# Optimization experiments

Hardware: AMD Instinct MI355X
Metric: run time of the kernel (lower is better)

Reference implementation:

```python
import jax, jax.numpy as jnp
import numpy as np

B, N, IN, OUT = 16, 1000, 128, 128


def setup_inputs() -> dict:
    key = jax.random.key(0)
    ks = jax.random.split(key, 8)
    stdv = 1.0 / np.sqrt(IN + OUT)  # matches reset_param uniform(-stdv, stdv)
    def w(k):
        return jax.random.uniform(k, (N, IN + OUT, OUT), jnp.float32, -stdv, stdv)
    return {
        "xt": jax.random.normal(ks[0], (B, N, IN), jnp.float32),
        "hidden": jax.random.normal(ks[1], (1, N, OUT), jnp.float32),
        "ct_1": jax.random.normal(ks[2], (1, N, OUT), jnp.float32),
        "W_i": w(ks[3]), "b_i": jnp.zeros((N, OUT), jnp.float32),
        "W_o": w(ks[4]), "b_o": jnp.zeros((N, OUT), jnp.float32),
        "W_f": w(ks[5]), "b_f": jnp.zeros((N, OUT), jnp.float32),
        "W_c": w(ks[6]), "b_c": jnp.zeros((N, OUT), jnp.float32),
    }


def reference(xt, hidden, ct_1, W_i, b_i, W_o, b_o, W_f, b_f, W_c, b_c):
    b = xt.shape[0]
    h = jnp.broadcast_to(hidden, (b,) + hidden.shape[1:])       # [B,N,OUT]
    xh = jnp.concatenate([xt, h], axis=-1)                      # [B,N,IN+OUT]

    def gate(W, bias, act):
        # per-stock batched matmul: [B,N,K] x [N,K,O] -> [B,N,O]
        return act(jnp.einsum('bnk,nko->bno', xh, W) + bias)

    it = gate(W_i, b_i, jax.nn.sigmoid)
    ot = gate(W_o, b_o, jax.nn.sigmoid)
    ft = gate(W_f, b_f, jax.nn.sigmoid)
    chat = gate(W_c, b_c, jnp.tanh)

    ct = ft * jnp.broadcast_to(ct_1, it.shape) + it * chat
    ht = ot * jnp.tanh(ct)
    return ht, ct
```

## Files before the change

### kernel.cpp

```cpp
#include <hip/hip_runtime.h>
#include <hip/hip_bf16.h>

namespace {
constexpr int B   = 16;
constexpr int NS  = 1000;
constexpr int IN  = 128;
constexpr int OUT = 128;
constexpr int K   = 256;

typedef __attribute__((ext_vector_type(8))) short short8;
typedef __attribute__((ext_vector_type(4))) float f32x4;

__device__ __forceinline__ float fsigmoid(float x) {
  return 1.0f / (1.0f + __expf(-x));
}
__device__ __forceinline__ float ftanh(float x) {
  return 2.0f / (1.0f + __expf(-2.0f * x)) - 1.0f;
}
__device__ __forceinline__ unsigned int f2bf(float f) {
  unsigned int u = __builtin_bit_cast(unsigned int, f);
  u += 0x7fffu + ((u >> 16) & 1u);
  return u >> 16;
}
__device__ __forceinline__ unsigned int pack2(float lo, float hi) {
  return f2bf(lo) | (f2bf(hi) << 16);
}
__device__ __forceinline__ int slice_addr(int base, int kq, int col) {
  return base + (kq << 10) + ((col << 4) ^ (((col >> 3) & 7) << 4));
}

__global__ __launch_bounds__(512, 2) void lstm_kernel(
    const float* __restrict__ xt, const float* __restrict__ hidden,
    const float* __restrict__ ct_1,
    const float* __restrict__ Wi, const float* __restrict__ bi,
    const float* __restrict__ Wo, const float* __restrict__ bo,
    const float* __restrict__ Wf, const float* __restrict__ bfp,
    const float* __restrict__ Wc, const float* __restrict__ bc,
    float* __restrict__ out) {
  __shared__ __align__(16) unsigned char smem[40960];

  const int n   = blockIdx.x;
  const int tid = threadIdx.x;

  {
    const int b  = tid >> 5;
    const int s  = tid & 31;
    const int k0 = s << 3;
    float v[8];
    if (k0 < IN) {
      const float4 a = *reinterpret_cast<const float4*>(xt + ((size_t)b * NS + n) * IN + k0);
      const float4 c = *reinterpret_cast<const float4*>(xt + ((size_t)b * NS + n) * IN + k0 + 4);
      v[0]=a.x; v[1]=a.y; v[2]=a.z; v[3]=a.w; v[4]=c.x; v[5]=c.y; v[6]=c.z; v[7]=c.w;
    } else {
      const float4 a = *reinterpret_cast<const float4*>(hidden + (size_t)n * OUT + (k0 - IN));
      const float4 c = *reinterpret_cast<const float4*>(hidden + (size_t)n * OUT + (k0 - IN) + 4);
      v[0]=a.x; v[1]=a.y; v[2]=a.z; v[3]=a.w; v[4]=c.x; v[5]=c.y; v[6]=c.z; v[7]=c.w;
    }
    uint4 pk;
    pk.x = pack2(v[0], v[1]); pk.y = pack2(v[2], v[3]);
    pk.z = pack2(v[4], v[5]); pk.w = pack2(v[6], v[7]);
    const int addr = ((b << 9) + (s << 4)) ^ ((b & 7) << 4);
    *reinterpret_cast<uint4*>(&smem[addr]) = pk;
  }
  __syncthreads();

  const int wid  = tid >> 6;
  const int g    = wid >> 1;
  const int half = wid & 1;
  const int l    = tid & 63;
  const int g2   = l >> 4;
  const int c16  = l & 15;

  const float* Wg = (g == 0) ? Wi : (g == 1) ? Wo : (g == 2) ? Wf : Wc;
  const float* bg = (g == 0) ? bi : (g == 1) ? bo : (g == 2) ? bfp : bc;
  const float* wbase = Wg + (size_t)n * (K * OUT) + half * 64 + (c16 << 2);

  const int wsl = 8192 + (wid << 12);
  f32x4 acc[4] = {f32x4{0,0,0,0}, f32x4{0,0,0,0}, f32x4{0,0,0,0}, f32x4{0,0,0,0}};

  float4 wqa[8], wqb[8];
  #pragma unroll
  for (int i = 0; i < 8; ++i)
    wqa[i] = *reinterpret_cast<const float4*>(wbase + (size_t)((g2 << 3) + i) * OUT);
  #pragma unroll
  for (int i = 0; i < 8; ++i)
    wqb[i] = *reinterpret_cast<const float4*>(wbase + (size_t)(32 + (g2 << 3) + i) * OUT);

  #pragma unroll 1
  for (int c = 0; c < 8; c += 2) {
    {
      uint4 pk[4];
      #pragma unroll
      for (int j = 0; j < 4; ++j) {
        pk[j].x = pack2((&wqa[0].x)[j], (&wqa[1].x)[j]);
        pk[j].y = pack2((&wqa[2].x)[j], (&wqa[3].x)[j]);
        pk[j].z = pack2((&wqa[4].x)[j], (&wqa[5].x)[j]);
        pk[j].w = pack2((&wqa[6].x)[j], (&wqa[7].x)[j]);
      }
      const int cn = (c + 2 < 8) ? c + 2 : 0;
      #pragma unroll
      for (int i = 0; i < 8; ++i)
        wqa[i] = *reinterpret_cast<const float4*>(
            wbase + (size_t)((cn << 5) + (g2 << 3) + i) * OUT);
      #pragma unroll
      for (int j = 0; j < 4; ++j)
        *reinterpret_cast<uint4*>(&smem[slice_addr(wsl, g2, (c16 << 2) + j)]) = pk[j];

      const int aaddr = ((c16 << 9) + (c << 6) + (g2 << 4)) ^ ((c16 & 7) << 4);
      const short8 af = *reinterpret_cast<const short8*>(&smem[aaddr]);
      #pragma unroll
      for (int t = 0; t < 4; ++t) {
        const short8 bfv = *reinterpret_cast<const short8*>(
            &smem[slice_addr(wsl, g2, (t << 4) + c16)]);
        acc[t] = __builtin_amdgcn_mfma_f32_16x16x32_bf16(af, bfv, acc[t], 0, 0, 0);
      }
    }
    {
      uint4 pk[4];
      #pragma unroll
      for (int j = 0; j < 4; ++j) {
        pk[j].x = pack2((&wqb[0].x)[j], (&wqb[1].x)[j]);
        pk[j].y = pack2((&wqb[2].x)[j], (&wqb[3].x)[j]);
        pk[j].z = pack2((&wqb[4].x)[j], (&wqb[5].x)[j]);
        pk[j].w = pack2((&wqb[6].x)[j], (&wqb[7].x)[j]);
      }
      const int cn = (c + 3 < 8) ? c + 3 : 0;
      #pragma unroll
      for (int i = 0; i < 8; ++i)
        wqb[i] = *reinterpret_cast<const float4*>(
            wbase + (size_t)((cn << 5) + (g2 << 3) + i) * OUT);
      #pragma unroll
      for (int j = 0; j < 4; ++j)
        *reinterpret_cast<uint4*>(&smem[slice_addr(wsl, g2, (c16 << 2) + j)]) = pk[j];

      const int aaddr = ((c16 << 9) + ((c + 1) << 6) + (g2 << 4)) ^ ((c16 & 7) << 4);
      const short8 af = *reinterpret_cast<const short8*>(&smem[aaddr]);
      #pragma unroll
      for (int t = 0; t < 4; ++t) {
        const short8 bfv = *reinterpret_cast<const short8*>(
            &smem[slice_addr(wsl, g2, (t << 4) + c16)]);
        acc[t] = __builtin_amdgcn_mfma_f32_16x16x32_bf16(af, bfv, acc[t], 0, 0, 0);
      }
    }
  }

  __syncthreads();
  float* gb = reinterpret_cast<float*>(smem);
  #pragma unroll
  for (int t = 0; t < 4; ++t) {
    const int colg = (half << 6) + (t << 4) + c16;
    const float bias = bg[(size_t)n * OUT + colg];
    #pragma unroll
    for (int r = 0; r < 4; ++r) {
      const int b = (g2 << 2) + r;
      gb[g * 2064 + b * 129 + colg] = acc[t][r] + bias;
    }
  }
  __syncthreads();

  const size_t nbase = (size_t)n * OUT;
  #pragma unroll
  for (int r = 0; r < 4; ++r) {
    const int p = tid + (r << 9);
    const int b = p >> 7;
    const int o = p & 127;
    const float gi = gb[0 * 2064 + b * 129 + o];
    const float go = gb[1 * 2064 + b * 129 + o];
    const float gf = gb[2 * 2064 + b * 129 + o];
    const float gc = gb[3 * 2064 + b * 129 + o];
    const float it = fsigmoid(gi);
    const float ot = fsigmoid(go);
    const float ft = fsigmoid(gf);
    const float ch = ftanh(gc);
    const float cp = ct_1[nbase + o];
    const float ct = ft * cp + it * ch;
    const float ht = ot * ftanh(ct);
    const size_t oidx = (size_t)b * ((size_t)NS * OUT) + nbase + o;
    out[oidx] = ht;
    out[(size_t)B * NS * OUT + oidx] = ct;
  }
}
}

extern "C" void kernel_launch(void* const* d_in, const int* in_sizes, int n_in,
                              void* d_out, int out_size, void* d_ws, size_t ws_size,
                              hipStream_t stream) {
  const float* xt     = (const float*)d_in[0];
  const float* hidden = (const float*)d_in[1];
  const float* ct_1   = (const float*)d_in[2];
  const float* Wi     = (const float*)d_in[3];
  const float* bi     = (const float*)d_in[4];
  const float* Wo     = (const float*)d_in[5];
  const float* bo     = (const float*)d_in[6];
  const float* Wf     = (const float*)d_in[7];
  const float* bf     = (const float*)d_in[8];
  const float* Wc     = (const float*)d_in[9];
  const float* bc     = (const float*)d_in[10];

  lstm_kernel<<<NS, 512, 0, stream>>>(xt, hidden, ct_1, Wi, bi, Wo, bo,
                                      Wf, bf, Wc, bc,
                                      (float*)d_out);
}
```

Before: 110.6 us.

## Split each stock across two 256-thread blocks by output half

Each stock is now handled by two blocks, one per 64-column half of the output, with four waves (one per gate) instead of eight. The weight prefetch per step is halved: each wave loads 32 K-rows per iteration in two 16-row halves and does one MFMA step per iteration. Shared memory shrinks to 24 KB and launch bounds allow six blocks per CU, aiming for more occupancy and more blocks in flight to hide weight-streaming latency. In exchange, the activation tile (xt and hidden) is loaded and converted twice per stock, and each iteration now carries less independent memory work.

```diff
diff --git a/kernel.cpp b/kernel.cpp
--- a/kernel.cpp
+++ b/kernel.cpp
@@ -29,7 +29,7 @@
   return base + (kq << 10) + ((col << 4) ^ (((col >> 3) & 7) << 4));
 }
 
-__global__ __launch_bounds__(512, 2) void lstm_kernel(
+__global__ __launch_bounds__(256, 6) void lstm_kernel(
     const float* __restrict__ xt, const float* __restrict__ hidden,
     const float* __restrict__ ct_1,
     const float* __restrict__ Wi, const float* __restrict__ bi,
@@ -37,15 +37,19 @@
     const float* __restrict__ Wf, const float* __restrict__ bfp,
     const float* __restrict__ Wc, const float* __restrict__ bc,
     float* __restrict__ out) {
-  __shared__ __align__(16) unsigned char smem[40960];
+  __shared__ __align__(16) unsigned char smem[24576];
 
-  const int n   = blockIdx.x;
-  const int tid = threadIdx.x;
+  const int bid  = blockIdx.x;
+  const int n    = bid >> 1;
+  const int half = bid & 1;
+  const int tid  = threadIdx.x;
 
-  {
-    const int b  = tid >> 5;
-    const int s  = tid & 31;
-    const int k0 = s << 3;
+  #pragma unroll
+  for (int r = 0; r < 2; ++r) {
+    const int idx = tid + (r << 8);
+    const int b   = idx >> 5;
+    const int s   = idx & 31;
+    const int k0  = s << 3;
     float v[8];
     if (k0 < IN) {
       const float4 a = *reinterpret_cast<const float4*>(xt + ((size_t)b * NS + n) * IN + k0);
@@ -64,83 +68,73 @@
   }
   __syncthreads();
 
-  const int wid  = tid >> 6;
-  const int g    = wid >> 1;
-  const int half = wid & 1;
-  const int l    = tid & 63;
-  const int g2   = l >> 4;
-  const int c16  = l & 15;
+  const int g   = tid >> 6;
+  const int l   = tid & 63;
+  const int g2  = l >> 4;
+  const int c16 = l & 15;
 
   const float* Wg = (g == 0) ? Wi : (g == 1) ? Wo : (g == 2) ? Wf : Wc;
   const float* bg = (g == 0) ? bi : (g == 1) ? bo : (g == 2) ? bfp : bc;
   const float* wbase = Wg + (size_t)n * (K * OUT) + half * 64 + (c16 << 2);
 
-  const int wsl = 8192 + (wid << 12);
+  const int wsl = 8192 + (g << 12);
   f32x4 acc[4] = {f32x4{0,0,0,0}, f32x4{0,0,0,0}, f32x4{0,0,0,0}, f32x4{0,0,0,0}};
 
-  float4 wqa[8], wqb[8];
+  float4 wqa[4], wqb[4];
   #pragma unroll
-  for (int i = 0; i < 8; ++i)
-    wqa[i] = *reinterpret_cast<const float4*>(wbase + (size_t)((g2 << 3) + i) * OUT);
+  for (int i = 0; i < 4; ++i)
+    wqa[i] = *reinterpret_cast<const float4*>(wbase + (size_t)((g2 << 2) + i) * OUT);
   #pragma unroll
-  for (int i = 0; i < 8; ++i)
-    wqb[i] = *reinterpret_cast<const float4*>(wbase + (size_t)(32 + (g2 << 3) + i) * OUT);
+  for (int i = 0; i < 4; ++i)
+    wqb[i] = *reinterpret_cast<const float4*>(wbase + (size_t)(16 + (g2 << 2) + i) * OUT);
 
   #pragma unroll 1
-  for (int c = 0; c < 8; c += 2) {
+  for (int c = 0; c < 8; ++c) {
     {
-      uint4 pk[4];
+      uint2 pw[4];
       #pragma unroll
       for (int j = 0; j < 4; ++j) {
-        pk[j].x = pack2((&wqa[0].x)[j], (&wqa[1].x)[j]);
-        pk[j].y = pack2((&wqa[2].x)[j], (&wqa[3].x)[j]);
-        pk[j].z = pack2((&wqa[4].x)[j], (&wqa[5].x)[j]);
-        pk[j].w = pack2((&wqa[6].x)[j], (&wqa[7].x)[j]);
+        pw[j].x = pack2((&wqa[0].x)[j], (&wqa[1].x)[j]);
+        pw[j].y = pack2((&wqa[2].x)[j], (&wqa[3].x)[j]);
       }
-      const int cn = (c + 2 < 8) ? c + 2 : 0;
+      if (c < 7) {
+        #pragma unroll
+        for (int i = 0; i < 4; ++i)
+          wqa[i] = *reinterpret_cast<const float4*>(
+              wbase + (size_t)(((c + 1) << 5) + (g2 << 2) + i) * OUT);
+      }
       #pragma unroll
-      for (int i = 0; i < 8; ++i)
-        wqa[i] = *reinterpret_cast<const float4*>(
-            wbase + (size_t)((cn << 5) + (g2 << 3) + i) * OUT);
-      #pragma unroll
-      for (int j = 0; j < 4; ++j)
-        *reinterpret_cast<uint4*>(&smem[slice_addr(wsl, g2, (c16 << 2) + j)]) = pk[j];
-
-      const int aaddr = ((c16 << 9) + (c << 6) + (g2 << 4)) ^ ((c16 & 7) << 4);
-      const short8 af = *reinterpret_cast<const short8*>(&smem[aaddr]);
-      #pragma unroll
-      for (int t = 0; t < 4; ++t) {
-        const short8 bfv = *reinterpret_cast<const short8*>(
-            &smem[slice_addr(wsl, g2, (t << 4) + c16)]);
-        acc[t] = __builtin_amdgcn_mfma_f32_16x16x32_bf16(af, bfv, acc[t], 0, 0, 0);
+      for (int j = 0; j < 4; ++j) {
+        const int a = slice_addr(wsl, g2 >> 1, (c16 << 2) + j) + ((g2 & 1) << 3);
+        *reinterpret_cast<uint2*>(&smem[a]) = pw[j];
       }
     }
     {
-      uint4 pk[4];
+      uint2 pw[4];
       #pragma unroll
       for (int j = 0; j < 4; ++j) {
-        pk[j].x = pack2((&wqb[0].x)[j], (&wqb[1].x)[j]);
-        pk[j].y = pack2((&wqb[2].x)[j], (&wqb[3].x)[j]);
-        pk[j].z = pack2((&wqb[4].x)[j], (&wqb[5].x)[j]);
-        pk[j].w = pack2((&wqb[6].x)[j], (&wqb[7].x)[j]);
+        pw[j].x = pack2((&wqb[0].x)[j], (&wqb[1].x)[j]);
+        pw[j].y = pack2((&wqb[2].x)[j], (&wqb[3].x)[j]);
       }
-      const int cn = (c + 3 < 8) ? c + 3 : 0;
+      if (c < 7) {
+        #pragma unroll
+        for (int i = 0; i < 4; ++i)
+          wqb[i] = *reinterpret_cast<const float4*>(
+              wbase + (size_t)(((c + 1) << 5) + 16 + (g2 << 2) + i) * OUT);
+      }
       #pragma unroll
-      for (int i = 0; i < 8; ++i)
-        wqb[i] = *reinterpret_cast<const float4*>(
-            wbase + (size_t)((cn << 5) + (g2 << 3) + i) * OUT);
-      #pragma unroll
-      for (int j = 0; j < 4; ++j)
-        *reinterpret_cast<uint4*>(&smem[slice_addr(wsl, g2, (c16 << 2) + j)]) = pk[j];
-
-      const int aaddr = ((c16 << 9) + ((c + 1) << 6) + (g2 << 4)) ^ ((c16 & 7) << 4);
-      const short8 af = *reinterpret_cast<const short8*>(&smem[aaddr]);
-      #pragma unroll
-      for (int t = 0; t < 4; ++t) {
-        const short8 bfv = *reinterpret_cast<const short8*>(
-            &smem[slice_addr(wsl, g2, (t << 4) + c16)]);
-        acc[t] = __builtin_amdgcn_mfma_f32_16x16x32_bf16(af, bfv, acc[t], 0, 0, 0);
+      for (int j = 0; j < 4; ++j) {
+        const int a = slice_addr(wsl, 2 + (g2 >> 1), (c16 << 2) + j) + ((g2 & 1) << 3);
+        *reinterpret_cast<uint2*>(&smem[a]) = pw[j];
       }
+    }
+    const int aaddr = ((c16 << 9) + (c << 6) + (g2 << 4)) ^ ((c16 & 7) << 4);
+    const short8 af = *reinterpret_cast<const short8*>(&smem[aaddr]);
+    #pragma unroll
+    for (int t = 0; t < 4; ++t) {
+      const short8 bfv = *reinterpret_cast<const short8*>(
+          &smem[slice_addr(wsl, g2, (t << 4) + c16)]);
+      acc[t] = __builtin_amdgcn_mfma_f32_16x16x32_bf16(af, bfv, acc[t], 0, 0, 0);
     }
   }
 
@@ -148,12 +142,12 @@
   float* gb = reinterpret_cast<float*>(smem);
   #pragma unroll
   for (int t = 0; t < 4; ++t) {
-    const int colg = (half << 6) + (t << 4) + c16;
-    const float bias = bg[(size_t)n * OUT + colg];
+    const int coll = (t << 4) + c16;
+    const float bias = bg[(size_t)n * OUT + half * 64 + coll];
     #pragma unroll
     for (int r = 0; r < 4; ++r) {
       const int b = (g2 << 2) + r;
-      gb[g * 2064 + b * 129 + colg] = acc[t][r] + bias;
+      gb[g * 1040 + b * 65 + coll] = acc[t][r] + bias;
     }
   }
   __syncthreads();
@@ -161,13 +155,14 @@
   const size_t nbase = (size_t)n * OUT;
   #pragma unroll
   for (int r = 0; r < 4; ++r) {
-    const int p = tid + (r << 9);
-    const int b = p >> 7;
-    const int o = p & 127;
-    const float gi = gb[0 * 2064 + b * 129 + o];
-    const float go = gb[1 * 2064 + b * 129 + o];
-    const float gf = gb[2 * 2064 + b * 129 + o];
-    const float gc = gb[3 * 2064 + b * 129 + o];
+    const int p    = tid + (r << 8);
+    const int b    = p >> 6;
+    const int coll = p & 63;
+    const int o    = half * 64 + coll;
+    const float gi = gb[0 * 1040 + b * 65 + coll];
+    const float go = gb[1 * 1040 + b * 65 + coll];
+    const float gf = gb[2 * 1040 + b * 65 + coll];
+    const float gc = gb[3 * 1040 + b * 65 + coll];
     const float it = fsigmoid(gi);
     const float ot = fsigmoid(go);
     const float ft = fsigmoid(gf);
@@ -197,7 +192,7 @@
   const float* Wc     = (const float*)d_in[9];
   const float* bc     = (const float*)d_in[10];
 
-  lstm_kernel<<<NS, 512, 0, stream>>>(xt, hidden, ct_1, Wi, bi, Wo, bo,
-                                      Wf, bf, Wc, bc,
-                                      (float*)d_out);
+  lstm_kernel<<<2 * NS, 256, 0, stream>>>(xt, hidden, ct_1, Wi, bi, Wo, bo,
+                                          Wf, bf, Wc, bc,
+                                          (float*)d_out);
 }
```

Measured after the change: 123.1 us. 1.11x slower.
